# Kernel optimization log

Hardware: AMD Instinct MI355X
Metric: run time of the kernel (lower is better)

The kernel has to match this reference:

```python
import jax, jax.numpy as jnp
import numpy as np

CTX = (16, 16)          # rel_pos_ctx_size
N_HEADS = 12
HEAD_DIM = 64           # emb_dim // n_heads


def _make_rel_pos_ids(ctx):
    # Faithful replication of the torch buffer construction.
    rge = [2 * s - 1 for s in ctx]
    coords = np.stack(np.meshgrid(*[np.arange(s) for s in ctx], indexing='ij'))  # [2, *ctx]
    coords = coords.reshape(len(ctx), -1)                                        # [2, n]
    rel = coords[:, :, None] - coords[:, None, :]                                # [2, n, n]
    rel = rel.reshape(len(ctx), -1)                                              # [2, n*n]
    rel = rel + (np.array(ctx)[:, None] - 1)
    ids = np.ravel_multi_index(tuple(rel), tuple(rge))                           # [n*n]
    return jnp.asarray(ids, dtype=jnp.int32)


def setup_inputs() -> dict:
    key = jax.random.key(0)
    ks = jax.random.split(key, 6)
    b, n, e = 128, 256, 768
    std_in = 1.0 / np.sqrt(e)
    return {
        'x': jax.random.normal(ks[0], (b, n, e), jnp.float32),
        'W_qkv': jax.random.normal(ks[1], (e, 3 * e), jnp.float32) * std_in,
        'b_qkv': jax.random.normal(ks[2], (3 * e,), jnp.float32) * 0.02,
        'W_out': jax.random.normal(ks[3], (e, e), jnp.float32) * std_in,
        'b_out': jax.random.normal(ks[4], (e,), jnp.float32) * 0.02,
        'rel_bias_table': jax.random.normal(ks[5], ((2 * CTX[0] - 1) * (2 * CTX[1] - 1), N_HEADS), jnp.float32) * 0.02,
        'rel_pos_ids': _make_rel_pos_ids(CTX),
    }


def reference(x, W_qkv, b_qkv, W_out, b_out, rel_bias_table, rel_pos_ids):
    b, n, e = x.shape
    h, d = N_HEADS, HEAD_DIM
    scale = d ** -0.5
    # fused qkv projection: 'b n (k h d) -> k b h n d'
    qkv = (x @ W_qkv + b_qkv).reshape(b, n, 3, h, d)
    q, k, v = (jnp.transpose(qkv, (2, 0, 3, 1, 4))[i] for i in range(3))  # each [b h n d]
    # gathered relative-position bias: [n*n, h] -> [h, n, n]
    bias = rel_bias_table[rel_pos_ids].reshape(n, n, h).transpose(2, 0, 1)
    scores = jnp.einsum('bhnd,bhmd->bhnm', q, k) * scale + bias
    attn = jax.nn.softmax(scores, axis=-1)
    out = jnp.einsum('bhnm,bhmd->bhnd', attn, v)
    out = out.transpose(0, 2, 1, 3).reshape(b, n, e)  # 'b h n d -> b n (h d)'
    return out @ W_out + b_out
```

## Files before the change

kernel.cpp:

```cpp
#include <hip/hip_runtime.h>
#include <cstdint>
#include <cstddef>

typedef __bf16 bf16x8 __attribute__((ext_vector_type(8)));
typedef __bf16 bf16x4 __attribute__((ext_vector_type(4)));
typedef float f32x4 __attribute__((ext_vector_type(4)));
static_assert(sizeof(bf16x8) == 16, "bf16x8 must be 16B");
static_assert(sizeof(bf16x4) == 8, "bf16x4 must be 8B");
static_assert(sizeof(f32x4) == 16, "f32x4 must be 16B");

#define MFMA16(a, b, c) __builtin_amdgcn_mfma_f32_16x16x32_bf16((a), (b), (c), 0, 0, 0)
#define SBAR() __builtin_amdgcn_s_barrier()
#define LGKM0() asm volatile("s_waitcnt lgkmcnt(0)" ::: "memory")
#define VMCNT(n_) asm volatile("s_waitcnt vmcnt(" #n_ ")" ::: "memory")

__device__ __forceinline__ void gload_lds16(const void* g, void* l) {
  __builtin_amdgcn_global_load_lds(
      (const __attribute__((address_space(1))) void*)g,
      (__attribute__((address_space(3))) void*)l, 16, 0, 0);
}

__global__ __launch_bounds__(256) void conv_x_kernel(const float* __restrict__ in,
                                                     __bf16* __restrict__ out) {
  size_t i = ((size_t)blockIdx.x * 256 + threadIdx.x) * 4;
  const float4 v = *(const float4*)(in + i);
  bf16x4 pk;
  pk[0] = (__bf16)v.x;
  pk[1] = (__bf16)v.y;
  pk[2] = (__bf16)v.z;
  pk[3] = (__bf16)v.w;
  *(bf16x4*)(out + i) = pk;
}

__global__ __launch_bounds__(256) void transpose_conv_kernel(const float* __restrict__ in,
                                                             __bf16* __restrict__ out,
                                                             int K, int N) {
  __shared__ float tile[32][33];
  const int n0 = blockIdx.x * 32, k0 = blockIdx.y * 32;
  const int tx = threadIdx.x, ty = threadIdx.y;
#pragma unroll
  for (int i = 0; i < 4; ++i)
    tile[ty * 4 + i][tx] = in[(size_t)(k0 + ty * 4 + i) * N + n0 + tx];
  __syncthreads();
#pragma unroll
  for (int i = 0; i < 4; ++i)
    out[(size_t)(n0 + ty * 4 + i) * K + k0 + tx] = (__bf16)tile[tx][ty * 4 + i];
}

__global__ __launch_bounds__(256) void bias_gather_kernel(const float* __restrict__ table,
                                                          const int* __restrict__ ids,
                                                          float* __restrict__ biasT) {
  const int idx = blockIdx.x * 256 + threadIdx.x;
  const int h = idx >> 16, ji = idx & 65535;
  const int j = ji >> 8, i = ji & 255;
  biasT[idx] = table[ids[i * 256 + j] * 12 + h];
}

template <int NT>
__global__ __launch_bounds__(512, 2) void gemm8_qkv_kernel(const __bf16* __restrict__ A,
                                                           const __bf16* __restrict__ Bt,
                                                           const float* __restrict__ bias,
                                                           __bf16* __restrict__ qb,
                                                           __bf16* __restrict__ kb,
                                                           __bf16* __restrict__ vt,
                                                           const int M, const int K) {
  __shared__ __align__(16) __bf16 smem[65536];
  const int tid = threadIdx.x;
  const int lane = tid & 63, w = tid >> 6;
  const int m16 = lane & 15, q4 = lane >> 4;
  const int wm = w & 1, wn = w >> 1;

  const int nwg = NT * (M >> 8);
  const int chunk = nwg >> 3;
  const int id = blockIdx.x;
  const int wg = (id & 7) * chunk + (id >> 3);
  const int mi = wg / NT, ni = wg - mi * NT;
  const int m0 = mi << 8, n0 = ni << 8;

  const int srow = w * 8 + (lane >> 3);
  const int sg = ((lane & 7) ^ (srow & 7)) * 8;
  const __bf16* ag = A + (size_t)(m0 + srow) * K + sg;
  const __bf16* bg = Bt + (size_t)(n0 + srow) * K + sg;
  const int dstw = w * 512;

  const int g0 = (q4 ^ (m16 & 7)) * 8;
  const int g1 = ((4 + q4) ^ (m16 & 7)) * 8;
  const int abase = (wm * 128 + m16) * 64;
  const int bbase = 16384 + (wn * 64 + m16) * 64;

  const int nt = K >> 6;

#define STAGE(T_, mat_, h_)                                                         \
  do {                                                                              \
    const __bf16* s_ = ((mat_) ? bg : ag) + (size_t)(T_)*64 + (size_t)(h_)*128 * K; \
    __bf16* d_ = &smem[((T_)&1) * 32768 + (mat_)*16384 + (h_)*8192 + dstw];         \
    gload_lds16(s_, d_);                                                            \
    gload_lds16(s_ + (size_t)64 * K, d_ + 4096);                                    \
  } while (0)

  STAGE(0, 0, 0);
  STAGE(0, 0, 1);
  STAGE(0, 1, 0);
  STAGE(0, 1, 1);
  STAGE(1, 0, 0);
  VMCNT(2);
  SBAR();

  f32x4 acc[8][4] = {};
  for (int T = 0; T < nt; ++T) {
    const int base = (T & 1) * 32768;
    bf16x8 a[4][2], b0[2][2], b1[2][2];

#pragma unroll
    for (int fm = 0; fm < 4; ++fm) {
      a[fm][0] = *(const bf16x8*)&smem[base + abase + fm * 1024 + g0];
      a[fm][1] = *(const bf16x8*)&smem[base + abase + fm * 1024 + g1];
    }
#pragma unroll
    for (int fn = 0; fn < 2; ++fn) {
      b0[fn][0] = *(const bf16x8*)&smem[base + bbase + fn * 1024 + g0];
      b0[fn][1] = *(const bf16x8*)&smem[base + bbase + fn * 1024 + g1];
    }
    if (T + 1 < nt) STAGE(T + 1, 0, 1);
    SBAR();
    LGKM0();
    __builtin_amdgcn_s_setprio(1);
#pragma unroll
    for (int kh = 0; kh < 2; ++kh)
#pragma unroll
      for (int fm = 0; fm < 4; ++fm)
#pragma unroll
        for (int fn = 0; fn < 2; ++fn)
          acc[fm][fn] = MFMA16(b0[fn][kh], a[fm][kh], acc[fm][fn]);
    __builtin_amdgcn_s_setprio(0);
    SBAR();

#pragma unroll
    for (int fn = 0; fn < 2; ++fn) {
      b1[fn][0] = *(const bf16x8*)&smem[base + bbase + 2048 + fn * 1024 + g0];
      b1[fn][1] = *(const bf16x8*)&smem[base + bbase + 2048 + fn * 1024 + g1];
    }
    if (T + 1 < nt) {
      STAGE(T + 1, 1, 0);
      STAGE(T + 1, 1, 1);
    }
    SBAR();
    LGKM0();
    __builtin_amdgcn_s_setprio(1);
#pragma unroll
    for (int kh = 0; kh < 2; ++kh)
#pragma unroll
      for (int fm = 0; fm < 4; ++fm)
#pragma unroll
        for (int fn = 0; fn < 2; ++fn)
          acc[fm][2 + fn] = MFMA16(b1[fn][kh], a[fm][kh], acc[fm][2 + fn]);
    __builtin_amdgcn_s_setprio(0);
    SBAR();

#pragma unroll
    for (int fm = 0; fm < 4; ++fm) {
      a[fm][0] = *(const bf16x8*)&smem[base + abase + 4096 + fm * 1024 + g0];
      a[fm][1] = *(const bf16x8*)&smem[base + abase + 4096 + fm * 1024 + g1];
    }
    SBAR();
    LGKM0();
    __builtin_amdgcn_s_setprio(1);
#pragma unroll
    for (int kh = 0; kh < 2; ++kh)
#pragma unroll
      for (int fm = 0; fm < 4; ++fm)
#pragma unroll
        for (int fn = 0; fn < 2; ++fn)
          acc[4 + fm][2 + fn] = MFMA16(b1[fn][kh], a[fm][kh], acc[4 + fm][2 + fn]);
    __builtin_amdgcn_s_setprio(0);
    SBAR();

    if (T + 2 < nt) {
      STAGE(T + 2, 0, 0);
      VMCNT(2);
    } else if (T + 1 < nt) {
      VMCNT(0);
    }
    SBAR();
    __builtin_amdgcn_s_setprio(1);
#pragma unroll
    for (int kh = 0; kh < 2; ++kh)
#pragma unroll
      for (int fm = 0; fm < 4; ++fm)
#pragma unroll
        for (int fn = 0; fn < 2; ++fn)
          acc[4 + fm][fn] = MFMA16(b0[fn][kh], a[fm][kh], acc[4 + fm][fn]);
    __builtin_amdgcn_s_setprio(0);
    SBAR();
  }
#undef STAGE

  __syncthreads();
  const int bi = m0 >> 8;
  char* eb = (char*)smem;

  if (n0 < 1536) {
    const int which = (n0 >= 768);
    const float qscale = which ? 1.0f : 0.125f;
#pragma unroll
    for (int fn = 0; fn < 4; ++fn) {
      const int nloc = wn * 64 + fn * 16 + q4 * 4;
      const f32x4 bn = *(const f32x4*)&bias[n0 + nloc];
      const int cb = nloc * 2;
      const int slot = cb >> 4;
      const int half8 = cb & 15;
#pragma unroll
      for (int fm = 0; fm < 8; ++fm) {
        const int tok = wm * 128 + fm * 16 + m16;
        bf16x4 pk;
#pragma unroll
        for (int r = 0; r < 4; ++r) pk[r] = (__bf16)((acc[fm][fn][r] + bn[r]) * qscale);
        *(bf16x4*)(eb + tok * 512 + ((slot ^ (tok & 7)) << 4) + half8) = pk;
      }
    }
    __syncthreads();
    const int nrel0 = n0 - which * 768;
    __bf16* dst = (which ? kb : qb) + (size_t)bi * 12 * 16384;
#pragma unroll
    for (int pass = 0; pass < 16; ++pass) {
      const int tokr = pass * 16 + (tid >> 5);
      const int slot = tid & 31;
      const bf16x8 vv = *(const bf16x8*)(eb + tokr * 512 + ((slot ^ (tokr & 7)) << 4));
      const int nr = nrel0 + slot * 8;
      *(bf16x8*)(dst + (size_t)(nr >> 6) * 16384 + (size_t)tokr * 64 + (nr & 63)) = vv;
    }
  } else {
#pragma unroll
    for (int fn = 0; fn < 4; ++fn)
#pragma unroll
      for (int r = 0; r < 4; ++r) {
        const int nloc = wn * 64 + fn * 16 + q4 * 4 + r;
        const float bn = bias[n0 + nloc];
#pragma unroll
        for (int fm = 0; fm < 8; ++fm) {
          const int tok = wm * 128 + fm * 16 + m16;
          const int tcb = tok * 2;
          *(__bf16*)(eb + nloc * 512 + (((tcb >> 4) ^ (nloc & 7)) << 4) + (tcb & 15)) =
              (__bf16)(acc[fm][fn][r] + bn);
        }
      }
    __syncthreads();
    const int nrel0v = n0 - 1536;
#pragma unroll
    for (int pass = 0; pass < 16; ++pass) {
      const int nr = pass * 16 + (tid >> 5);
      const int slot = tid & 31;
      const bf16x8 vv = *(const bf16x8*)(eb + nr * 512 + ((slot ^ (nr & 7)) << 4));
      const int ng = nrel0v + nr;
      *(bf16x8*)(vt + (((size_t)bi * 12 + (ng >> 6)) * 64 + (ng & 63)) * 256 + slot * 8) = vv;
    }
  }
}

template <int NT>
__global__ __launch_bounds__(512, 2) void gemm8_out_kernel(const __bf16* __restrict__ A,
                                                           const __bf16* __restrict__ Bt,
                                                           const float* __restrict__ bias,
                                                           float* __restrict__ out,
                                                           const int M, const int N,
                                                           const int K) {
  __shared__ __align__(16) __bf16 smem[65536];
  const int tid = threadIdx.x;
  const int lane = tid & 63, w = tid >> 6;
  const int m16 = lane & 15, q4 = lane >> 4;
  const int wm = w & 1, wn = w >> 1;

  const int nwg = NT * (M >> 8);
  const int chunk = nwg >> 3;
  const int id = blockIdx.x;
  const int wg = (id & 7) * chunk + (id >> 3);
  const int mi = wg / NT, ni = wg - mi * NT;
  const int m0 = mi << 8, n0 = ni << 8;

  const int srow = w * 8 + (lane >> 3);
  const int sg = ((lane & 7) ^ (srow & 7)) * 8;
  const __bf16* ag = A + (size_t)(m0 + srow) * K + sg;
  const __bf16* bg = Bt + (size_t)(n0 + srow) * K + sg;
  const int dstw = w * 512;

  const int g0 = (q4 ^ (m16 & 7)) * 8;
  const int g1 = ((4 + q4) ^ (m16 & 7)) * 8;
  const int abase = (wm * 128 + m16) * 64;
  const int bbase = 16384 + (wn * 64 + m16) * 64;

  const int nt = K >> 6;

#define STAGE(T_, mat_, h_)                                                         \
  do {                                                                              \
    const __bf16* s_ = ((mat_) ? bg : ag) + (size_t)(T_)*64 + (size_t)(h_)*128 * K; \
    __bf16* d_ = &smem[((T_)&1) * 32768 + (mat_)*16384 + (h_)*8192 + dstw];         \
    gload_lds16(s_, d_);                                                            \
    gload_lds16(s_ + (size_t)64 * K, d_ + 4096);                                    \
  } while (0)

  STAGE(0, 0, 0);
  STAGE(0, 0, 1);
  STAGE(0, 1, 0);
  STAGE(0, 1, 1);
  STAGE(1, 0, 0);
  VMCNT(2);
  SBAR();

  f32x4 acc[8][4] = {};
  for (int T = 0; T < nt; ++T) {
    const int base = (T & 1) * 32768;
    bf16x8 a[4][2], b0[2][2], b1[2][2];

#pragma unroll
    for (int fm = 0; fm < 4; ++fm) {
      a[fm][0] = *(const bf16x8*)&smem[base + abase + fm * 1024 + g0];
      a[fm][1] = *(const bf16x8*)&smem[base + abase + fm * 1024 + g1];
    }
#pragma unroll
    for (int fn = 0; fn < 2; ++fn) {
      b0[fn][0] = *(const bf16x8*)&smem[base + bbase + fn * 1024 + g0];
      b0[fn][1] = *(const bf16x8*)&smem[base + bbase + fn * 1024 + g1];
    }
    if (T + 1 < nt) STAGE(T + 1, 0, 1);
    SBAR();
    LGKM0();
    __builtin_amdgcn_s_setprio(1);
#pragma unroll
    for (int kh = 0; kh < 2; ++kh)
#pragma unroll
      for (int fm = 0; fm < 4; ++fm)
#pragma unroll
        for (int fn = 0; fn < 2; ++fn)
          acc[fm][fn] = MFMA16(b0[fn][kh], a[fm][kh], acc[fm][fn]);
    __builtin_amdgcn_s_setprio(0);
    SBAR();

#pragma unroll
    for (int fn = 0; fn < 2; ++fn) {
      b1[fn][0] = *(const bf16x8*)&smem[base + bbase + 2048 + fn * 1024 + g0];
      b1[fn][1] = *(const bf16x8*)&smem[base + bbase + 2048 + fn * 1024 + g1];
    }
    if (T + 1 < nt) {
      STAGE(T + 1, 1, 0);
      STAGE(T + 1, 1, 1);
    }
    SBAR();
    LGKM0();
    __builtin_amdgcn_s_setprio(1);
#pragma unroll
    for (int kh = 0; kh < 2; ++kh)
#pragma unroll
      for (int fm = 0; fm < 4; ++fm)
#pragma unroll
        for (int fn = 0; fn < 2; ++fn)
          acc[fm][2 + fn] = MFMA16(b1[fn][kh], a[fm][kh], acc[fm][2 + fn]);
    __builtin_amdgcn_s_setprio(0);
    SBAR();

#pragma unroll
    for (int fm = 0; fm < 4; ++fm) {
      a[fm][0] = *(const bf16x8*)&smem[base + abase + 4096 + fm * 1024 + g0];
      a[fm][1] = *(const bf16x8*)&smem[base + abase + 4096 + fm * 1024 + g1];
    }
    SBAR();
    LGKM0();
    __builtin_amdgcn_s_setprio(1);
#pragma unroll
    for (int kh = 0; kh < 2; ++kh)
#pragma unroll
      for (int fm = 0; fm < 4; ++fm)
#pragma unroll
        for (int fn = 0; fn < 2; ++fn)
          acc[4 + fm][2 + fn] = MFMA16(b1[fn][kh], a[fm][kh], acc[4 + fm][2 + fn]);
    __builtin_amdgcn_s_setprio(0);
    SBAR();

    if (T + 2 < nt) {
      STAGE(T + 2, 0, 0);
      VMCNT(2);
    } else if (T + 1 < nt) {
      VMCNT(0);
    }
    SBAR();
    __builtin_amdgcn_s_setprio(1);
#pragma unroll
    for (int kh = 0; kh < 2; ++kh)
#pragma unroll
      for (int fm = 0; fm < 4; ++fm)
#pragma unroll
        for (int fn = 0; fn < 2; ++fn)
          acc[4 + fm][fn] = MFMA16(b0[fn][kh], a[fm][kh], acc[4 + fm][fn]);
    __builtin_amdgcn_s_setprio(0);
    SBAR();
  }
#undef STAGE

  __syncthreads();
  char* ef = (char*)smem;
#pragma unroll
  for (int half = 0; half < 2; ++half) {
    if ((wn >> 1) == half) {
#pragma unroll
      for (int fn = 0; fn < 4; ++fn) {
        const int nl = (wn & 1) * 64 + fn * 16 + q4 * 4;
        const f32x4 bn = *(const f32x4*)&bias[n0 + half * 128 + nl];
        const int slot = nl >> 2;
#pragma unroll
        for (int fm = 0; fm < 8; ++fm) {
          const int tok = wm * 128 + fm * 16 + m16;
          f32x4 v;
#pragma unroll
          for (int r = 0; r < 4; ++r) v[r] = acc[fm][fn][r] + bn[r];
          *(f32x4*)(ef + tok * 512 + ((slot ^ (tok & 7)) << 4)) = v;
        }
      }
    }
    __syncthreads();
#pragma unroll
    for (int pass = 0; pass < 16; ++pass) {
      const int tokr = pass * 16 + (tid >> 5);
      const int slot = tid & 31;
      const f32x4 vv = *(const f32x4*)(ef + tokr * 512 + ((slot ^ (tokr & 7)) << 4));
      *(f32x4*)(out + (size_t)(m0 + tokr) * N + n0 + half * 128 + slot * 4) = vv;
    }
    __syncthreads();
  }
}

__global__ __launch_bounds__(512, 4) void attn_kernel(const __bf16* __restrict__ qb,
                                                      const __bf16* __restrict__ kb,
                                                      const __bf16* __restrict__ vtb,
                                                      const float* __restrict__ biasT,
                                                      __bf16* __restrict__ o_ws) {
  __shared__ __bf16 klds[256 * 64];
  __shared__ __bf16 vlds[64 * 256];
  const int tid = threadIdx.x;
  const int lane = tid & 63, w = tid >> 6;
  const int m16 = lane & 15, q4 = lane >> 4;
  const int b = blockIdx.x, h = blockIdx.y;
  const size_t bh = (size_t)b * 12 + h;
  const __bf16* Q = qb + bh * (256 * 64);
  const __bf16* Kp = kb + bh * (256 * 64);
  const __bf16* Vt = vtb + bh * (64 * 256);
  const float* BhT = biasT + (size_t)h * 65536;
  const int qbase = blockIdx.z * 128;
  const int qrow0 = qbase + w * 16;

#pragma unroll
  for (int i = 0; i < 4; ++i) {
    const int row = w * 32 + i * 8 + (lane >> 3);
    const int col = ((lane & 7) ^ (row & 7)) * 8;
    gload_lds16(Kp + (size_t)row * 64 + col, &klds[(w * 32 + i * 8) * 64]);
  }
#pragma unroll
  for (int i = 0; i < 4; ++i) {
    const int row = w * 8 + i * 2 + (lane >> 5);
    const int g = lane & 31;
    const int gp = (g & 24) | ((g & 7) ^ (row & 7));
    gload_lds16(Vt + (size_t)row * 256 + gp * 8, &vlds[(w * 8 + i * 2) * 256]);
  }

  bf16x8 qf[2];
#pragma unroll
  for (int t = 0; t < 2; ++t)
    qf[t] = *(const bf16x8*)(Q + (size_t)(qrow0 + m16) * 64 + t * 32 + q4 * 8);

  __syncthreads();

  f32x4 s[16];
#pragma unroll
  for (int c = 0; c < 16; ++c) {
    const int krow = c * 16 + m16;
    const bf16x8 kf0 = *(const bf16x8*)&klds[krow * 64 + ((q4 ^ (m16 & 7)) * 8)];
    const bf16x8 kf1 = *(const bf16x8*)&klds[krow * 64 + (((4 + q4) ^ (m16 & 7)) * 8)];
    f32x4 z = {0.f, 0.f, 0.f, 0.f};
    z = MFMA16(qf[0], kf0, z);
    s[c] = MFMA16(qf[1], kf1, z);
  }

#pragma unroll
  for (int c = 0; c < 16; ++c) {
    const f32x4 bv = *(const f32x4*)&BhT[(size_t)(c * 16 + m16) * 256 + qrow0 + q4 * 4];
    s[c] += bv;
  }

  float linv[4];
#pragma unroll
  for (int r = 0; r < 4; ++r) {
    float mx = s[0][r];
#pragma unroll
    for (int c = 1; c < 16; ++c) mx = fmaxf(mx, s[c][r]);
    mx = fmaxf(mx, __shfl_xor(mx, 1));
    mx = fmaxf(mx, __shfl_xor(mx, 2));
    mx = fmaxf(mx, __shfl_xor(mx, 4));
    mx = fmaxf(mx, __shfl_xor(mx, 8));
    float sum = 0.f;
#pragma unroll
    for (int c = 0; c < 16; ++c) {
      const float p = exp2f((s[c][r] - mx) * 1.4426950408889634f);
      s[c][r] = p;
      sum += p;
    }
    sum += __shfl_xor(sum, 1);
    sum += __shfl_xor(sum, 2);
    sum += __shfl_xor(sum, 4);
    sum += __shfl_xor(sum, 8);
    linv[r] = 1.f / sum;
  }

  __syncthreads();

  f32x4 o[4] = {};
  __bf16* P = &klds[w * 1152];
#pragma unroll
  for (int ch = 0; ch < 4; ++ch) {
#pragma unroll
    for (int cc = 0; cc < 4; ++cc)
#pragma unroll
      for (int r = 0; r < 4; ++r)
        P[(q4 * 4 + r) * 72 + cc * 16 + m16] = (__bf16)s[ch * 4 + cc][r];
#pragma unroll
    for (int kt = 0; kt < 2; ++kt) {
      const bf16x8 pf = *(const bf16x8*)(P + m16 * 72 + kt * 32 + q4 * 8);
#pragma unroll
      for (int dt = 0; dt < 4; ++dt) {
        const int vrow = dt * 16 + m16;
        const bf16x8 vf = *(const bf16x8*)&vlds[vrow * 256 + ch * 64 +
                                                (((kt * 4 + q4) ^ (m16 & 7)) * 8)];
        o[dt] = MFMA16(pf, vf, o[dt]);
      }
    }
  }

#pragma unroll
  for (int dt = 0; dt < 4; ++dt)
#pragma unroll
    for (int r = 0; r < 4; ++r) {
      const float v = o[dt][r] * linv[r];
      const size_t row = (size_t)b * 256 + qrow0 + q4 * 4 + r;
      o_ws[row * 768 + h * 64 + dt * 16 + m16] = (__bf16)v;
    }
}

extern "C" void kernel_launch(void* const* d_in, const int* in_sizes, int n_in,
                              void* d_out, int out_size, void* d_ws, size_t ws_size,
                              hipStream_t stream) {
  const float* x = (const float*)d_in[0];
  const float* Wqkv = (const float*)d_in[1];
  const float* bqkv = (const float*)d_in[2];
  const float* Wout = (const float*)d_in[3];
  const float* bout = (const float*)d_in[4];
  const float* table = (const float*)d_in[5];
  const int* ids = (const int*)d_in[6];
  float* out = (float*)d_out;

  char* ws = (char*)d_ws;
  __bf16* xbf = (__bf16*)ws;
  __bf16* wqkvt = (__bf16*)(ws + 50331648);
  __bf16* woutt = (__bf16*)(ws + 53870592);
  __bf16* qbuf = (__bf16*)(ws + 55050240);
  __bf16* kbuf = (__bf16*)(ws + 105381888);
  __bf16* vtbuf = (__bf16*)(ws + 155713536);
  float* biasT = (float*)(ws + 206045184);

  conv_x_kernel<<<24576, 256, 0, stream>>>(x, xbf);
  transpose_conv_kernel<<<dim3(72, 24), dim3(32, 8), 0, stream>>>(Wqkv, wqkvt, 768, 2304);
  transpose_conv_kernel<<<dim3(24, 24), dim3(32, 8), 0, stream>>>(Wout, woutt, 768, 768);
  bias_gather_kernel<<<3072, 256, 0, stream>>>(table, ids, biasT);
  gemm8_qkv_kernel<9><<<1152, 512, 0, stream>>>(xbf, wqkvt, bqkv, qbuf, kbuf, vtbuf,
                                                32768, 768);
  attn_kernel<<<dim3(128, 12, 2), 512, 0, stream>>>(qbuf, kbuf, vtbuf, biasT, xbf );
  gemm8_out_kernel<3><<<384, 512, 0, stream>>>(xbf, woutt, bout, out, 32768, 768, 768);
}
```

Baseline: 475.1 us.

## Merge prep kernels, issue all next-tile stages earlier, use native exp2

Folds the x conversion, both weight transposes and the bias gather into one prep kernel dispatched by block index, removing three launches. In both GEMMs, all three remaining stage loads for the next K tile are issued together before the first MFMA phase instead of being split across phases, so more global-to-LDS traffic overlaps with compute. The softmax uses the hardware exp2 builtin in place of exp2f. Issuing the stages earlier raises the number of outstanding loads, and the later VMCNT waits were tuned for the old split, so the pipelining may not line up as intended.

```diff
diff --git a/kernel.cpp b/kernel.cpp
--- a/kernel.cpp
+++ b/kernel.cpp
@@ -20,40 +20,47 @@
       (__attribute__((address_space(3))) void*)l, 16, 0, 0);
 }
 
-__global__ __launch_bounds__(256) void conv_x_kernel(const float* __restrict__ in,
-                                                     __bf16* __restrict__ out) {
-  size_t i = ((size_t)blockIdx.x * 256 + threadIdx.x) * 4;
-  const float4 v = *(const float4*)(in + i);
-  bf16x4 pk;
-  pk[0] = (__bf16)v.x;
-  pk[1] = (__bf16)v.y;
-  pk[2] = (__bf16)v.z;
-  pk[3] = (__bf16)v.w;
-  *(bf16x4*)(out + i) = pk;
-}
-
-__global__ __launch_bounds__(256) void transpose_conv_kernel(const float* __restrict__ in,
-                                                             __bf16* __restrict__ out,
-                                                             int K, int N) {
+__global__ __launch_bounds__(256) void prep_kernel(
+    const float* __restrict__ x, __bf16* __restrict__ xbf,
+    const float* __restrict__ Wqkv, __bf16* __restrict__ wqkvt,
+    const float* __restrict__ Wout, __bf16* __restrict__ woutt,
+    const float* __restrict__ table, const int* __restrict__ ids,
+    float* __restrict__ biasT) {
   __shared__ float tile[32][33];
-  const int n0 = blockIdx.x * 32, k0 = blockIdx.y * 32;
-  const int tx = threadIdx.x, ty = threadIdx.y;
-#pragma unroll
-  for (int i = 0; i < 4; ++i)
-    tile[ty * 4 + i][tx] = in[(size_t)(k0 + ty * 4 + i) * N + n0 + tx];
-  __syncthreads();
-#pragma unroll
-  for (int i = 0; i < 4; ++i)
-    out[(size_t)(n0 + ty * 4 + i) * K + k0 + tx] = (__bf16)tile[tx][ty * 4 + i];
-}
-
-__global__ __launch_bounds__(256) void bias_gather_kernel(const float* __restrict__ table,
-                                                          const int* __restrict__ ids,
-                                                          float* __restrict__ biasT) {
-  const int idx = blockIdx.x * 256 + threadIdx.x;
-  const int h = idx >> 16, ji = idx & 65535;
-  const int j = ji >> 8, i = ji & 255;
-  biasT[idx] = table[ids[i * 256 + j] * 12 + h];
+  const int bid = blockIdx.x;
+  const int tid = threadIdx.x;
+
+  if (bid < 24576) {
+    size_t i = ((size_t)bid * 256 + tid) * 4;
+    const float4 v = *(const float4*)(x + i);
+    bf16x4 pk;
+    pk[0] = (__bf16)v.x;
+    pk[1] = (__bf16)v.y;
+    pk[2] = (__bf16)v.z;
+    pk[3] = (__bf16)v.w;
+    *(bf16x4*)(xbf + i) = pk;
+  } else if (bid < 26880) {
+    const bool big = bid < 26304;
+    const int b2 = big ? (bid - 24576) : (bid - 26304);
+    const int nt = big ? 72 : 24;
+    const int N = big ? 2304 : 768;
+    const float* in = big ? Wqkv : Wout;
+    __bf16* out = big ? wqkvt : woutt;
+    const int n0 = (b2 % nt) * 32, k0 = (b2 / nt) * 32;
+    const int tx = tid & 31, ty = tid >> 5;
+#pragma unroll
+    for (int i = 0; i < 4; ++i)
+      tile[ty * 4 + i][tx] = in[(size_t)(k0 + ty * 4 + i) * N + n0 + tx];
+    __syncthreads();
+#pragma unroll
+    for (int i = 0; i < 4; ++i)
+      out[(size_t)(n0 + ty * 4 + i) * 768 + k0 + tx] = (__bf16)tile[tx][ty * 4 + i];
+  } else {
+    const int idx = (bid - 26880) * 256 + tid;
+    const int h = idx >> 16, ji = idx & 65535;
+    const int j = ji >> 8, i = ji & 255;
+    biasT[idx] = table[ids[i * 256 + j] * 12 + h];
+  }
 }
 
 template <int NT>
@@ -121,7 +128,11 @@
       b0[fn][0] = *(const bf16x8*)&smem[base + bbase + fn * 1024 + g0];
       b0[fn][1] = *(const bf16x8*)&smem[base + bbase + fn * 1024 + g1];
     }
-    if (T + 1 < nt) STAGE(T + 1, 0, 1);
+    if (T + 1 < nt) {
+      STAGE(T + 1, 0, 1);
+      STAGE(T + 1, 1, 0);
+      STAGE(T + 1, 1, 1);
+    }
     SBAR();
     LGKM0();
     __builtin_amdgcn_s_setprio(1);
@@ -139,10 +150,6 @@
     for (int fn = 0; fn < 2; ++fn) {
       b1[fn][0] = *(const bf16x8*)&smem[base + bbase + 2048 + fn * 1024 + g0];
       b1[fn][1] = *(const bf16x8*)&smem[base + bbase + 2048 + fn * 1024 + g1];
-    }
-    if (T + 1 < nt) {
-      STAGE(T + 1, 1, 0);
-      STAGE(T + 1, 1, 1);
     }
     SBAR();
     LGKM0();
@@ -321,7 +328,11 @@
       b0[fn][0] = *(const bf16x8*)&smem[base + bbase + fn * 1024 + g0];
       b0[fn][1] = *(const bf16x8*)&smem[base + bbase + fn * 1024 + g1];
     }
-    if (T + 1 < nt) STAGE(T + 1, 0, 1);
+    if (T + 1 < nt) {
+      STAGE(T + 1, 0, 1);
+      STAGE(T + 1, 1, 0);
+      STAGE(T + 1, 1, 1);
+    }
     SBAR();
     LGKM0();
     __builtin_amdgcn_s_setprio(1);
@@ -339,10 +350,6 @@
     for (int fn = 0; fn < 2; ++fn) {
       b1[fn][0] = *(const bf16x8*)&smem[base + bbase + 2048 + fn * 1024 + g0];
       b1[fn][1] = *(const bf16x8*)&smem[base + bbase + 2048 + fn * 1024 + g1];
-    }
-    if (T + 1 < nt) {
-      STAGE(T + 1, 1, 0);
-      STAGE(T + 1, 1, 1);
     }
     SBAR();
     LGKM0();
@@ -497,7 +504,7 @@
     float sum = 0.f;
 #pragma unroll
     for (int c = 0; c < 16; ++c) {
-      const float p = exp2f((s[c][r] - mx) * 1.4426950408889634f);
+      const float p = __builtin_amdgcn_exp2f((s[c][r] - mx) * 1.4426950408889634f);
       s[c][r] = p;
       sum += p;
     }
@@ -563,10 +570,8 @@
   __bf16* vtbuf = (__bf16*)(ws + 155713536);
   float* biasT = (float*)(ws + 206045184);
 
-  conv_x_kernel<<<24576, 256, 0, stream>>>(x, xbf);
-  transpose_conv_kernel<<<dim3(72, 24), dim3(32, 8), 0, stream>>>(Wqkv, wqkvt, 768, 2304);
-  transpose_conv_kernel<<<dim3(24, 24), dim3(32, 8), 0, stream>>>(Wout, woutt, 768, 768);
-  bias_gather_kernel<<<3072, 256, 0, stream>>>(table, ids, biasT);
+  prep_kernel<<<29952, 256, 0, stream>>>(x, xbf, Wqkv, wqkvt, Wout, woutt,
+                                         table, ids, biasT);
   gemm8_qkv_kernel<9><<<1152, 512, 0, stream>>>(xbf, wqkvt, bqkv, qbuf, kbuf, vtbuf,
                                                 32768, 768);
   attn_kernel<<<dim3(128, 12, 2), 512, 0, stream>>>(qbuf, kbuf, vtbuf, biasT, xbf );
```

Result: faster. 460.3 us (-3.1%).
